# Kernel optimization log

Hardware: AMD Instinct MI355X
Metric: run time of the kernel (lower is better)

Reference implementation:

```python
import jax, jax.numpy as jnp
import numpy as np

H = 224; W = 224; ZNEAR = 0.01; ZFAR = 100.0; EPS2D = 0.3
N_GAUSS = 1024; N_CAM = 2
ALPHA_MIN = 1.0 / 255.0; ALPHA_MAX = 0.999


def quat_to_rotmat(q):
    # gsplat convention: wxyz, normalized internally. q: [N,4] -> [N,3,3]
    q = q / jnp.linalg.norm(q, axis=-1, keepdims=True)
    w, x, y, z = q[:, 0], q[:, 1], q[:, 2], q[:, 3]
    R = jnp.stack([
        jnp.stack([1.0 - 2.0 * (y * y + z * z), 2.0 * (x * y - w * z), 2.0 * (x * z + w * y)], -1),
        jnp.stack([2.0 * (x * y + w * z), 1.0 - 2.0 * (x * x + z * z), 2.0 * (y * z - w * x)], -1),
        jnp.stack([2.0 * (x * z - w * y), 2.0 * (y * z + w * x), 1.0 - 2.0 * (x * x + y * y)], -1),
    ], -2)
    return R


def setup_inputs() -> dict:
    key = jax.random.key(0)
    ks = jax.random.split(key, 5)
    xyz = jax.random.normal(ks[0], (N_GAUSS, 3), dtype=jnp.float32) * 0.5
    rgb = jax.random.uniform(ks[1], (N_GAUSS, 3), dtype=jnp.float32)
    opacity = jax.random.uniform(ks[2], (N_GAUSS,), dtype=jnp.float32)
    scale = jax.random.uniform(ks[3], (N_GAUSS, 3), dtype=jnp.float32) * 0.04 + 0.005
    rotation = jax.random.normal(ks[4], (N_GAUSS, 4), dtype=jnp.float32)
    w2c_list = []
    for a in (0.0, 0.3):  # two views, small yaw apart, camera 3 units back
        c, s = np.cos(a), np.sin(a)
        w2c_list.append(np.array([[c, 0, -s, 0], [0, 1, 0, 0], [s, 0, c, 3.0], [0, 0, 0, 1]], dtype=np.float32))
    w2cs = jnp.asarray(np.stack(w2c_list))
    K = np.array([[300.0, 0.0, 112.0], [0.0, 300.0, 112.0], [0.0, 0.0, 1.0]], dtype=np.float32)
    Ks = jnp.asarray(np.stack([K] * N_CAM))
    return {"w2cs": w2cs, "Ks": Ks, "xyz": xyz, "rgb": rgb, "opacity": opacity, "scale": scale, "rotation": rotation}


def _render_one(viewmat, K, means, cov3d, colors, opac, bg):
    R = viewmat[:3, :3]; t = viewmat[:3, 3]
    p_cam = means @ R.T + t                       # [N,3]
    z = p_cam[:, 2]; rz = 1.0 / z
    fx, fy, cx, cy = K[0, 0], K[1, 1], K[0, 2], K[1, 2]
    lim_x = 1.3 * (0.5 * W / fx); lim_y = 1.3 * (0.5 * H / fy)
    tx = z * jnp.clip(p_cam[:, 0] * rz, -lim_x, lim_x)
    ty = z * jnp.clip(p_cam[:, 1] * rz, -lim_y, lim_y)
    # camera-frame 3D covariance, then perspective Jacobian projection to 2D
    cov_cam = jnp.einsum('ij,njk,lk->nil', R, cov3d, R)   # [N,3,3]
    zero = jnp.zeros_like(rz)
    J = jnp.stack([
        jnp.stack([fx * rz, zero, -fx * tx * rz * rz], -1),
        jnp.stack([zero, fy * rz, -fy * ty * rz * rz], -1),
    ], -2)                                                # [N,2,3]
    cov2d = jnp.einsum('nij,njk,nlk->nil', J, cov_cam, J) # [N,2,2]
    a = cov2d[:, 0, 0] + EPS2D; d = cov2d[:, 1, 1] + EPS2D; b = cov2d[:, 0, 1]
    det = a * d - b * b
    ia = d / det; id_ = a / det; ib = -b / det            # inverse of blurred 2D cov
    u = fx * p_cam[:, 0] * rz + cx
    v = fy * p_cam[:, 1] * rz + cy
    valid = (z > ZNEAR) & (z < ZFAR) & (det > 0)
    o = jnp.where(valid, opac, 0.0)
    # front-to-back depth sort (gradients flow through gathered values)
    order = jnp.argsort(z)
    u, v, ia, ib, id_, o = (arr[order] for arr in (u, v, ia, ib, id_, o))
    colors_s = colors[order]
    # pixel centers, row-major flattened grid [P]
    xs = jnp.arange(W, dtype=jnp.float32) + 0.5
    ys = jnp.arange(H, dtype=jnp.float32) + 0.5
    pix_x = jnp.tile(xs, H); pix_y = jnp.repeat(ys, W)
    dx = u[None, :] - pix_x[:, None]                      # [P,N]
    dy = v[None, :] - pix_y[:, None]
    sigma = 0.5 * (ia * dx * dx + id_ * dy * dy) + ib * dx * dy
    alpha = jnp.minimum(o[None, :] * jnp.exp(-sigma), ALPHA_MAX)
    alpha = jnp.where((sigma >= 0.0) & (alpha > ALPHA_MIN), alpha, 0.0)
    log1m = jnp.log1p(-alpha)
    logT = jnp.cumsum(log1m, axis=1)
    T = jnp.exp(logT - log1m)                             # exclusive transmittance
    wgt = alpha * T                                       # [P,N]
    img = wgt @ colors_s                                  # [P,3]
    Tf = jnp.exp(logT[:, -1])
    img = img + Tf[:, None] * bg
    return img.reshape(H, W, 3), (1.0 - Tf).reshape(H, W, 1)


def reference(w2cs, Ks, xyz, rgb, opacity, scale, rotation):
    Rq = quat_to_rotmat(rotation)                         # [N,3,3]
    M = Rq * scale[:, None, :]                            # R @ diag(s)
    cov3d = jnp.einsum('nij,nkj->nik', M, M)              # R S S^T R^T
    bg = jnp.ones((3,), dtype=xyz.dtype)                  # bg_color buffer of ones
    imgs, alphas = jax.vmap(lambda vm, K: _render_one(vm, K, xyz, cov3d, rgb, opacity, bg))(w2cs, Ks)
    return imgs, alphas                                   # rgb [C,H,W,3], mask [C,H,W,1]
```

## Files before the change

kernel.cpp:

```cpp
#include <hip/hip_runtime.h>
#include <math.h>

#define NG 1024
#define NC 2
#define HH 224
#define WW 224
#define TILES_X 28
#define TILES_Y 28
#define EPS2D 0.3f
#define ALPHA_MIN (1.0f/255.0f)
#define ALPHA_MAX 0.999f
#define MAXL 512
#define LOG2E 1.4426950408889634f

__global__ __launch_bounds__(256) void fused_kernel(
        const float* __restrict__ w2cs, const float* __restrict__ Ks,
        const float* __restrict__ xyz, const float* __restrict__ rgb,
        const float* __restrict__ opac, const float* __restrict__ scale,
        const float* __restrict__ rot, float* __restrict__ out) {
    const int cam = blockIdx.z;
    const int TX = blockIdx.x, TY = blockIdx.y;
    const int tid = threadIdx.x;
    const int lane = tid & 63;
    const int wv   = tid >> 6;

    __shared__ union {
        unsigned long long keys[MAXL];
        float4 part[4][64];
    } shu;
    __shared__ float4 sA[MAXL];
    __shared__ float4 sB[MAXL];
    __shared__ float  sC[MAXL];
    __shared__ int    cnt[8];
    __shared__ int    scnt;

    if (tid == 0) scnt = 0;
    __syncthreads();

    const float* vm = w2cs + cam*16;
    const float R00 = vm[0],  R01 = vm[1],  R02 = vm[2],  t0 = vm[3];
    const float R10 = vm[4],  R11 = vm[5],  R12 = vm[6],  t1 = vm[7];
    const float R20 = vm[8],  R21 = vm[9],  R22 = vm[10], t2 = vm[11];
    const float* Kc = Ks + cam*9;
    const float fx = Kc[0], cx = Kc[2], fy = Kc[4], cy = Kc[5];
    const float limx = 1.3f * (0.5f * (float)WW / fx);
    const float limy = 1.3f * (0.5f * (float)HH / fy);

    #pragma unroll
    for (int k = 0; k < 4; k++) {
        int g = k*256 + tid;
        float X = xyz[g*3], Y = xyz[g*3+1], Z = xyz[g*3+2];
        float pz = R20*X + R21*Y + R22*Z + t2;
        float o  = opac[g];
        float tau = __logf(255.f * o);
        bool cand = (pz > 0.01f) && (pz < 100.f) && (tau > 0.f);
        if (cand) {
            float rz = 1.f / pz;
            float px = R00*X + R01*Y + R02*Z + t0;
            float py = R10*X + R11*Y + R12*Z + t1;
            float uu = fx*px*rz + cx;
            float vv = fy*py*rz + cy;
            float sx = scale[g*3+0], sy = scale[g*3+1], sz = scale[g*3+2];
            float smax = fmaxf(sx, fmaxf(sy, sz));
            float j00 = fx*rz, j11 = fy*rz;
            float j02m = fx*limx*rz, j12m = fy*limy*rz;
            float abnd = smax*smax*(j00*j00 + j02m*j02m) + EPS2D;
            float dbnd = smax*smax*(j11*j11 + j12m*j12m) + EPS2D;
            float rx = sqrtf(2.f*tau*abnd) + 0.01f;
            float ry = sqrtf(2.f*tau*dbnd) + 0.01f;
            int xmin = max((int)ceilf (uu - rx - 0.5f), 0);
            int xmax = min((int)floorf(uu + rx - 0.5f), WW-1);
            int ymin = max((int)ceilf (vv - ry - 0.5f), 0);
            int ymax = min((int)floorf(vv + ry - 0.5f), HH-1);
            cand = (xmin <= xmax) && (ymin <= ymax) &&
                   (TX >= (xmin>>3)) && (TX <= (xmax>>3)) &&
                   (TY >= (ymin>>3)) && (TY <= (ymax>>3));
        }
        unsigned long long m = __ballot(cand);
        int cw = __popcll(m);
        if (cw) {
            int basepos = 0;
            if (lane == 0) basepos = atomicAdd(&scnt, cw);
            basepos = __shfl(basepos, 0);
            if (cand) {
                int pos = basepos + __popcll(m & ((1ull << lane) - 1ull));
                if (pos < MAXL)
                    shu.keys[pos] = ((unsigned long long)__float_as_uint(pz) << 10)
                                  | (unsigned long long)g;
            }
        }
    }
    __syncthreads();
    int n = min(scnt, MAXL);

    unsigned long long myk0 = (tid       < n) ? shu.keys[tid]       : 0ull;
    unsigned long long myk1 = (tid + 256 < n) ? shu.keys[tid + 256] : 0ull;
    int r0 = 0, r1 = 0;
    #pragma unroll 4
    for (int j = 0; j < n; j++) {
        unsigned long long kj = shu.keys[j];
        r0 += (kj < myk0) ? 1 : 0;
        r1 += (kj < myk1) ? 1 : 0;
    }
    __syncthreads();
    if (tid       < n) shu.keys[r0] = myk0;
    if (tid + 256 < n) shu.keys[r1] = myk1;
    __syncthreads();

    auto prep = [&](int i, float4 &A, float4 &B, float &C) -> bool {
        if (i >= n) return false;
        int g = (int)(shu.keys[i] & 1023ull);

        float qw = rot[g*4+0], qx = rot[g*4+1], qy = rot[g*4+2], qz = rot[g*4+3];
        float qn = rsqrtf(qw*qw + qx*qx + qy*qy + qz*qz);
        qw *= qn; qx *= qn; qy *= qn; qz *= qn;
        float r00 = 1.f - 2.f*(qy*qy + qz*qz), r01 = 2.f*(qx*qy - qw*qz), r02 = 2.f*(qx*qz + qw*qy);
        float r10 = 2.f*(qx*qy + qw*qz), r11 = 1.f - 2.f*(qx*qx + qz*qz), r12 = 2.f*(qy*qz - qw*qx);
        float r20 = 2.f*(qx*qz - qw*qy), r21 = 2.f*(qy*qz + qw*qx), r22 = 1.f - 2.f*(qx*qx + qy*qy);

        float sx = scale[g*3+0], sy = scale[g*3+1], sz = scale[g*3+2];
        float m00 = r00*sx, m01 = r01*sy, m02 = r02*sz;
        float m10 = r10*sx, m11 = r11*sy, m12 = r12*sz;
        float m20 = r20*sx, m21 = r21*sy, m22 = r22*sz;
        float c00 = m00*m00 + m01*m01 + m02*m02;
        float c01 = m00*m10 + m01*m11 + m02*m12;
        float c02 = m00*m20 + m01*m21 + m02*m22;
        float c11 = m10*m10 + m11*m11 + m12*m12;
        float c12 = m10*m20 + m11*m21 + m12*m22;
        float c22 = m20*m20 + m21*m21 + m22*m22;

        float X = xyz[g*3], Y = xyz[g*3+1], Z = xyz[g*3+2];
        float px = R00*X + R01*Y + R02*Z + t0;
        float py = R10*X + R11*Y + R12*Z + t1;
        float pz = R20*X + R21*Y + R22*Z + t2;
        float rz = 1.f / pz;

        float txc = pz * fminf(fmaxf(px*rz, -limx), limx);
        float tyc = pz * fminf(fmaxf(py*rz, -limy), limy);

        float v00 = R00*c00 + R01*c01 + R02*c02;
        float v01 = R00*c01 + R01*c11 + R02*c12;
        float v02 = R00*c02 + R01*c12 + R02*c22;
        float v10 = R10*c00 + R11*c01 + R12*c02;
        float v11 = R10*c01 + R11*c11 + R12*c12;
        float v12 = R10*c02 + R11*c12 + R12*c22;
        float v20 = R20*c00 + R21*c01 + R22*c02;
        float v21 = R20*c01 + R21*c11 + R22*c12;
        float v22 = R20*c02 + R21*c12 + R22*c22;
        float cc00 = v00*R00 + v01*R01 + v02*R02;
        float cc01 = v00*R10 + v01*R11 + v02*R12;
        float cc02 = v00*R20 + v01*R21 + v02*R22;
        float cc11 = v10*R10 + v11*R11 + v12*R12;
        float cc12 = v10*R20 + v11*R21 + v12*R22;
        float cc22 = v20*R20 + v21*R21 + v22*R22;

        float j00 = fx*rz, j02 = -fx*txc*rz*rz;
        float j11 = fy*rz, j12 = -fy*tyc*rz*rz;
        float a  = j00*j00*cc00 + 2.f*j00*j02*cc02 + j02*j02*cc22 + EPS2D;
        float bq = j00*j11*cc01 + j00*j12*cc02 + j02*j11*cc12 + j02*j12*cc22;
        float d  = j11*j11*cc11 + 2.f*j11*j12*cc12 + j12*j12*cc22 + EPS2D;
        float det = a*d - bq*bq;

        if (!((pz > 0.01f) && (pz < 100.f) && (det > 0.f))) return false;

        float o = opac[g];
        float tau = __logf(255.f * o);
        if (!(tau > 0.f)) return false;

        float hx = sqrtf(2.f*tau*a) + 0.02f;
        float hy = sqrtf(2.f*tau*d) + 0.02f;
        float uu = fx*px*rz + cx;
        float vv = fy*py*rz + cy;
        float xlo = (float)(TX*8) + 0.5f, xhi = (float)(TX*8) + 7.5f;
        float ylo = (float)(TY*8) + 0.5f, yhi = (float)(TY*8) + 7.5f;
        if (uu + hx < xlo || uu - hx > xhi || vv + hy < ylo || vv - hy > yhi)
            return false;

        float idet = 1.f / det;
        A = make_float4(uu, vv, 0.5f*LOG2E*d*idet, -LOG2E*bq*idet);
        B = make_float4(0.5f*LOG2E*a*idet, o, rgb[g*3+0], rgb[g*3+1]);
        C = rgb[g*3+2];
        return true;
    };

    float4 A0, B0, A1, B1; float C0, C1;
    bool kp0 = prep(tid,       A0, B0, C0);
    bool kp1 = prep(tid + 256, A1, B1, C1);

    unsigned long long bal0 = __ballot(kp0);
    unsigned long long bal1 = __ballot(kp1);
    if (lane == 0) { cnt[wv] = __popcll(bal0); cnt[4 + wv] = __popcll(bal1); }
    __syncthreads();
    int base0 = 0, base1 = 0, n2 = 0;
    #pragma unroll
    for (int s = 0; s < 8; s++) {
        int cs = cnt[s];
        base0 += (s < wv)     ? cs : 0;
        base1 += (s < 4 + wv) ? cs : 0;
        n2 += cs;
    }
    unsigned long long lt = (1ull << lane) - 1ull;
    int d0 = base0 + __popcll(bal0 & lt);
    int d1 = base1 + __popcll(bal1 & lt);
    if (kp0) { sA[d0] = A0; sB[d0] = B0; sC[d0] = C0; }
    if (kp1) { sA[d1] = A1; sB[d1] = B1; sC[d1] = C1; }
    __syncthreads();

    const float pxl = (float)(TX*8 + (lane & 7)) + 0.5f;
    const float pyl = (float)(TY*8 + (lane >> 3)) + 0.5f;
    int seglen = (n2 + 3) >> 2;
    int js = wv * seglen;
    int je = min(n2, js + seglen);

    float T = 1.f, cr = 0.f, cg = 0.f, cb = 0.f;
#define CBODY(J) do { \
        float4 ga = sA[J]; float4 gb = sB[J]; float bv = sC[J]; \
        float dx = ga.x - pxl, dy = ga.y - pyl; \
        float sg = ga.z*dx*dx + gb.x*dy*dy + ga.w*dx*dy; \
        float al = fminf(gb.y * exp2f(-sg), ALPHA_MAX); \
        al = (sg >= 0.f && al > ALPHA_MIN) ? al : 0.f; \
        float wgt = al * T; \
        cr += wgt * gb.z; cg += wgt * gb.w; cb += wgt * bv; \
        T -= al * T; \
    } while (0)

    int j = js;
    while (j + 16 <= je) {
        #pragma unroll 4
        for (int q = 0; q < 16; q++) { CBODY(j + q); }
        j += 16;
        if (__all(T < 1e-4f)) break;
    }
    for (; j < je; j++) { CBODY(j); }
#undef CBODY

    shu.part[wv][lane] = make_float4(cr, cg, cb, T);
    __syncthreads();

    if (tid < 64) {
        float4 c0 = shu.part[0][lane];
        float Cr = c0.x, Cg = c0.y, Cb = c0.z, Tp = c0.w;
        #pragma unroll
        for (int s = 1; s < 4; s++) {
            float4 cs = shu.part[s][lane];
            Cr += Tp * cs.x;
            Cg += Tp * cs.y;
            Cb += Tp * cs.z;
            Tp *= cs.w;
        }
        int p = (TY*8 + (lane >> 3)) * WW + TX*8 + (lane & 7);
        float* img = out + (size_t)cam * (HH*WW*3) + (size_t)p * 3;
        img[0] = Cr + Tp;
        img[1] = Cg + Tp;
        img[2] = Cb + Tp;
        out[(size_t)NC*HH*WW*3 + (size_t)cam*(HH*WW) + p] = 1.f - Tp;
    }
}

extern "C" void kernel_launch(void* const* d_in, const int* in_sizes, int n_in,
                              void* d_out, int out_size, void* d_ws, size_t ws_size,
                              hipStream_t stream) {
    const float* w2cs  = (const float*)d_in[0];
    const float* Ks    = (const float*)d_in[1];
    const float* xyz   = (const float*)d_in[2];
    const float* rgb   = (const float*)d_in[3];
    const float* opac  = (const float*)d_in[4];
    const float* scale = (const float*)d_in[5];
    const float* rot   = (const float*)d_in[6];
    float* out = (float*)d_out;

    fused_kernel<<<dim3(TILES_X, TILES_Y, NC), 256, 0, stream>>>(
        w2cs, Ks, xyz, rgb, opac, scale, rot, out);
}
```

Baseline: 77.94 us.

## Split fused renderer into per-Gaussian prep, global depth sort, and tile render kernels

The fused kernel is split into three kernels. The first projects each Gaussian once per camera into a workspace, together with its tile bounding box and a depth key. The second computes a global depth rank per camera and scatters the records into sorted order. The render kernel then selects its Gaussians by a bounding-box test, so each tile no longer repeats the projection and the O(n^2) local sort. This adds two kernel launches and global-memory round trips, and the tighter per-Gaussian bounds may change which Gaussians each tile includes.

New measurement: 90.03 us. +15.5%, slower.

```diff
diff --git a/kernel.cpp b/kernel.cpp
--- a/kernel.cpp
+++ b/kernel.cpp
@@ -13,29 +13,23 @@
 #define MAXL 512
 #define LOG2E 1.4426950408889634f
 
-__global__ __launch_bounds__(256) void fused_kernel(
+#define OFF_SA   0
+#define OFF_SB   (OFF_SA  + NC*NG*16)
+#define OFF_SC   (OFF_SB  + NC*NG*16)
+#define OFF_SBB  (OFF_SC  + NC*NG*4)
+#define OFF_KEY  (OFF_SBB + NC*NG*4)
+#define OFF_UA   (OFF_KEY + NC*NG*8)
+#define OFF_UB   (OFF_UA  + NC*NG*16)
+#define OFF_UC   (OFF_UB  + NC*NG*16)
+#define OFF_UBB  (OFF_UC  + NC*NG*4)
+
+__global__ __launch_bounds__(256) void prep_kernel(
         const float* __restrict__ w2cs, const float* __restrict__ Ks,
         const float* __restrict__ xyz, const float* __restrict__ rgb,
         const float* __restrict__ opac, const float* __restrict__ scale,
-        const float* __restrict__ rot, float* __restrict__ out) {
-    const int cam = blockIdx.z;
-    const int TX = blockIdx.x, TY = blockIdx.y;
-    const int tid = threadIdx.x;
-    const int lane = tid & 63;
-    const int wv   = tid >> 6;
-
-    __shared__ union {
-        unsigned long long keys[MAXL];
-        float4 part[4][64];
-    } shu;
-    __shared__ float4 sA[MAXL];
-    __shared__ float4 sB[MAXL];
-    __shared__ float  sC[MAXL];
-    __shared__ int    cnt[8];
-    __shared__ int    scnt;
-
-    if (tid == 0) scnt = 0;
-    __syncthreads();
+        const float* __restrict__ rot, unsigned char* __restrict__ ws) {
+    const int cam = blockIdx.y;
+    const int g = blockIdx.x * 256 + threadIdx.x;
 
     const float* vm = w2cs + cam*16;
     const float R00 = vm[0],  R01 = vm[1],  R02 = vm[2],  t0 = vm[3];
@@ -46,164 +40,181 @@
     const float limx = 1.3f * (0.5f * (float)WW / fx);
     const float limy = 1.3f * (0.5f * (float)HH / fy);
 
-    #pragma unroll
-    for (int k = 0; k < 4; k++) {
-        int g = k*256 + tid;
-        float X = xyz[g*3], Y = xyz[g*3+1], Z = xyz[g*3+2];
-        float pz = R20*X + R21*Y + R22*Z + t2;
-        float o  = opac[g];
-        float tau = __logf(255.f * o);
-        bool cand = (pz > 0.01f) && (pz < 100.f) && (tau > 0.f);
-        if (cand) {
-            float rz = 1.f / pz;
-            float px = R00*X + R01*Y + R02*Z + t0;
-            float py = R10*X + R11*Y + R12*Z + t1;
-            float uu = fx*px*rz + cx;
-            float vv = fy*py*rz + cy;
-            float sx = scale[g*3+0], sy = scale[g*3+1], sz = scale[g*3+2];
-            float smax = fmaxf(sx, fmaxf(sy, sz));
-            float j00 = fx*rz, j11 = fy*rz;
-            float j02m = fx*limx*rz, j12m = fy*limy*rz;
-            float abnd = smax*smax*(j00*j00 + j02m*j02m) + EPS2D;
-            float dbnd = smax*smax*(j11*j11 + j12m*j12m) + EPS2D;
-            float rx = sqrtf(2.f*tau*abnd) + 0.01f;
-            float ry = sqrtf(2.f*tau*dbnd) + 0.01f;
-            int xmin = max((int)ceilf (uu - rx - 0.5f), 0);
-            int xmax = min((int)floorf(uu + rx - 0.5f), WW-1);
-            int ymin = max((int)ceilf (vv - ry - 0.5f), 0);
-            int ymax = min((int)floorf(vv + ry - 0.5f), HH-1);
-            cand = (xmin <= xmax) && (ymin <= ymax) &&
-                   (TX >= (xmin>>3)) && (TX <= (xmax>>3)) &&
-                   (TY >= (ymin>>3)) && (TY <= (ymax>>3));
-        }
-        unsigned long long m = __ballot(cand);
-        int cw = __popcll(m);
-        if (cw) {
-            int basepos = 0;
-            if (lane == 0) basepos = atomicAdd(&scnt, cw);
-            basepos = __shfl(basepos, 0);
-            if (cand) {
-                int pos = basepos + __popcll(m & ((1ull << lane) - 1ull));
-                if (pos < MAXL)
-                    shu.keys[pos] = ((unsigned long long)__float_as_uint(pz) << 10)
-                                  | (unsigned long long)g;
-            }
-        }
-    }
-    __syncthreads();
-    int n = min(scnt, MAXL);
-
-    unsigned long long myk0 = (tid       < n) ? shu.keys[tid]       : 0ull;
-    unsigned long long myk1 = (tid + 256 < n) ? shu.keys[tid + 256] : 0ull;
-    int r0 = 0, r1 = 0;
-    #pragma unroll 4
-    for (int j = 0; j < n; j++) {
-        unsigned long long kj = shu.keys[j];
-        r0 += (kj < myk0) ? 1 : 0;
-        r1 += (kj < myk1) ? 1 : 0;
-    }
-    __syncthreads();
-    if (tid       < n) shu.keys[r0] = myk0;
-    if (tid + 256 < n) shu.keys[r1] = myk1;
-    __syncthreads();
-
-    auto prep = [&](int i, float4 &A, float4 &B, float &C) -> bool {
-        if (i >= n) return false;
-        int g = (int)(shu.keys[i] & 1023ull);
-
-        float qw = rot[g*4+0], qx = rot[g*4+1], qy = rot[g*4+2], qz = rot[g*4+3];
-        float qn = rsqrtf(qw*qw + qx*qx + qy*qy + qz*qz);
-        qw *= qn; qx *= qn; qy *= qn; qz *= qn;
-        float r00 = 1.f - 2.f*(qy*qy + qz*qz), r01 = 2.f*(qx*qy - qw*qz), r02 = 2.f*(qx*qz + qw*qy);
-        float r10 = 2.f*(qx*qy + qw*qz), r11 = 1.f - 2.f*(qx*qx + qz*qz), r12 = 2.f*(qy*qz - qw*qx);
-        float r20 = 2.f*(qx*qz - qw*qy), r21 = 2.f*(qy*qz + qw*qx), r22 = 1.f - 2.f*(qx*qx + qy*qy);
-
-        float sx = scale[g*3+0], sy = scale[g*3+1], sz = scale[g*3+2];
-        float m00 = r00*sx, m01 = r01*sy, m02 = r02*sz;
-        float m10 = r10*sx, m11 = r11*sy, m12 = r12*sz;
-        float m20 = r20*sx, m21 = r21*sy, m22 = r22*sz;
-        float c00 = m00*m00 + m01*m01 + m02*m02;
-        float c01 = m00*m10 + m01*m11 + m02*m12;
-        float c02 = m00*m20 + m01*m21 + m02*m22;
-        float c11 = m10*m10 + m11*m11 + m12*m12;
-        float c12 = m10*m20 + m11*m21 + m12*m22;
-        float c22 = m20*m20 + m21*m21 + m22*m22;
-
-        float X = xyz[g*3], Y = xyz[g*3+1], Z = xyz[g*3+2];
-        float px = R00*X + R01*Y + R02*Z + t0;
-        float py = R10*X + R11*Y + R12*Z + t1;
-        float pz = R20*X + R21*Y + R22*Z + t2;
-        float rz = 1.f / pz;
-
-        float txc = pz * fminf(fmaxf(px*rz, -limx), limx);
-        float tyc = pz * fminf(fmaxf(py*rz, -limy), limy);
-
-        float v00 = R00*c00 + R01*c01 + R02*c02;
-        float v01 = R00*c01 + R01*c11 + R02*c12;
-        float v02 = R00*c02 + R01*c12 + R02*c22;
-        float v10 = R10*c00 + R11*c01 + R12*c02;
-        float v11 = R10*c01 + R11*c11 + R12*c12;
-        float v12 = R10*c02 + R11*c12 + R12*c22;
-        float v20 = R20*c00 + R21*c01 + R22*c02;
-        float v21 = R20*c01 + R21*c11 + R22*c12;
-        float v22 = R20*c02 + R21*c12 + R22*c22;
-        float cc00 = v00*R00 + v01*R01 + v02*R02;
-        float cc01 = v00*R10 + v01*R11 + v02*R12;
-        float cc02 = v00*R20 + v01*R21 + v02*R22;
-        float cc11 = v10*R10 + v11*R11 + v12*R12;
-        float cc12 = v10*R20 + v11*R21 + v12*R22;
-        float cc22 = v20*R20 + v21*R21 + v22*R22;
-
-        float j00 = fx*rz, j02 = -fx*txc*rz*rz;
-        float j11 = fy*rz, j12 = -fy*tyc*rz*rz;
-        float a  = j00*j00*cc00 + 2.f*j00*j02*cc02 + j02*j02*cc22 + EPS2D;
-        float bq = j00*j11*cc01 + j00*j12*cc02 + j02*j11*cc12 + j02*j12*cc22;
-        float d  = j11*j11*cc11 + 2.f*j11*j12*cc12 + j12*j12*cc22 + EPS2D;
-        float det = a*d - bq*bq;
-
-        if (!((pz > 0.01f) && (pz < 100.f) && (det > 0.f))) return false;
-
-        float o = opac[g];
-        float tau = __logf(255.f * o);
-        if (!(tau > 0.f)) return false;
-
+    float qw = rot[g*4+0], qx = rot[g*4+1], qy = rot[g*4+2], qz = rot[g*4+3];
+    float qn = rsqrtf(qw*qw + qx*qx + qy*qy + qz*qz);
+    qw *= qn; qx *= qn; qy *= qn; qz *= qn;
+    float r00 = 1.f - 2.f*(qy*qy + qz*qz), r01 = 2.f*(qx*qy - qw*qz), r02 = 2.f*(qx*qz + qw*qy);
+    float r10 = 2.f*(qx*qy + qw*qz), r11 = 1.f - 2.f*(qx*qx + qz*qz), r12 = 2.f*(qy*qz - qw*qx);
+    float r20 = 2.f*(qx*qz - qw*qy), r21 = 2.f*(qy*qz + qw*qx), r22 = 1.f - 2.f*(qx*qx + qy*qy);
+
+    float sx = scale[g*3+0], sy = scale[g*3+1], sz = scale[g*3+2];
+    float m00 = r00*sx, m01 = r01*sy, m02 = r02*sz;
+    float m10 = r10*sx, m11 = r11*sy, m12 = r12*sz;
+    float m20 = r20*sx, m21 = r21*sy, m22 = r22*sz;
+    float c00 = m00*m00 + m01*m01 + m02*m02;
+    float c01 = m00*m10 + m01*m11 + m02*m12;
+    float c02 = m00*m20 + m01*m21 + m02*m22;
+    float c11 = m10*m10 + m11*m11 + m12*m12;
+    float c12 = m10*m20 + m11*m21 + m12*m22;
+    float c22 = m20*m20 + m21*m21 + m22*m22;
+
+    float X = xyz[g*3], Y = xyz[g*3+1], Z = xyz[g*3+2];
+    float px = R00*X + R01*Y + R02*Z + t0;
+    float py = R10*X + R11*Y + R12*Z + t1;
+    float pz = R20*X + R21*Y + R22*Z + t2;
+    float rz = 1.f / pz;
+
+    float txc = pz * fminf(fmaxf(px*rz, -limx), limx);
+    float tyc = pz * fminf(fmaxf(py*rz, -limy), limy);
+
+    float v00 = R00*c00 + R01*c01 + R02*c02;
+    float v01 = R00*c01 + R01*c11 + R02*c12;
+    float v02 = R00*c02 + R01*c12 + R02*c22;
+    float v10 = R10*c00 + R11*c01 + R12*c02;
+    float v11 = R10*c01 + R11*c11 + R12*c12;
+    float v12 = R10*c02 + R11*c12 + R12*c22;
+    float v20 = R20*c00 + R21*c01 + R22*c02;
+    float v21 = R20*c01 + R21*c11 + R22*c12;
+    float v22 = R20*c02 + R21*c12 + R22*c22;
+    float cc00 = v00*R00 + v01*R01 + v02*R02;
+    float cc01 = v00*R10 + v01*R11 + v02*R12;
+    float cc02 = v00*R20 + v01*R21 + v02*R22;
+    float cc11 = v10*R10 + v11*R11 + v12*R12;
+    float cc12 = v10*R20 + v11*R21 + v12*R22;
+    float cc22 = v20*R20 + v21*R21 + v22*R22;
+
+    float j00 = fx*rz, j02 = -fx*txc*rz*rz;
+    float j11 = fy*rz, j12 = -fy*tyc*rz*rz;
+    float a  = j00*j00*cc00 + 2.f*j00*j02*cc02 + j02*j02*cc22 + EPS2D;
+    float bq = j00*j11*cc01 + j00*j12*cc02 + j02*j11*cc12 + j02*j12*cc22;
+    float d  = j11*j11*cc11 + 2.f*j11*j12*cc12 + j12*j12*cc22 + EPS2D;
+    float det = a*d - bq*bq;
+
+    float o = opac[g];
+    float tau = __logf(255.f * o);
+    bool valid = (pz > 0.01f) && (pz < 100.f) && (det > 0.f) && (tau > 0.f);
+
+    float4 A4 = make_float4(0.f, 0.f, 0.f, 0.f);
+    float4 B4 = make_float4(0.f, 0.f, 0.f, 0.f);
+    float  C1 = 0.f;
+    unsigned bb = 0xFFFFFFFFu;
+    unsigned long long key = (0xFFFFFFFFull << 10) | (unsigned)g;
+
+    if (valid) {
         float hx = sqrtf(2.f*tau*a) + 0.02f;
         float hy = sqrtf(2.f*tau*d) + 0.02f;
         float uu = fx*px*rz + cx;
         float vv = fy*py*rz + cy;
-        float xlo = (float)(TX*8) + 0.5f, xhi = (float)(TX*8) + 7.5f;
-        float ylo = (float)(TY*8) + 0.5f, yhi = (float)(TY*8) + 7.5f;
-        if (uu + hx < xlo || uu - hx > xhi || vv + hy < ylo || vv - hy > yhi)
-            return false;
-
-        float idet = 1.f / det;
-        A = make_float4(uu, vv, 0.5f*LOG2E*d*idet, -LOG2E*bq*idet);
-        B = make_float4(0.5f*LOG2E*a*idet, o, rgb[g*3+0], rgb[g*3+1]);
-        C = rgb[g*3+2];
-        return true;
-    };
-
-    float4 A0, B0, A1, B1; float C0, C1;
-    bool kp0 = prep(tid,       A0, B0, C0);
-    bool kp1 = prep(tid + 256, A1, B1, C1);
-
-    unsigned long long bal0 = __ballot(kp0);
-    unsigned long long bal1 = __ballot(kp1);
-    if (lane == 0) { cnt[wv] = __popcll(bal0); cnt[4 + wv] = __popcll(bal1); }
-    __syncthreads();
-    int base0 = 0, base1 = 0, n2 = 0;
+        int xmin = max((int)ceilf (uu - hx - 0.5f), 0);
+        int xmax = min((int)floorf(uu + hx - 0.5f), WW-1);
+        int ymin = max((int)ceilf (vv - hy - 0.5f), 0);
+        int ymax = min((int)floorf(vv + hy - 0.5f), HH-1);
+        if (xmin <= xmax && ymin <= ymax) {
+            bb = (unsigned)(xmin>>3) | ((unsigned)(xmax>>3)<<8)
+               | ((unsigned)(ymin>>3)<<16) | ((unsigned)(ymax>>3)<<24);
+            float idet = 1.f / det;
+            A4 = make_float4(uu, vv, 0.5f*LOG2E*d*idet, -LOG2E*bq*idet);
+            B4 = make_float4(0.5f*LOG2E*a*idet, o, rgb[g*3+0], rgb[g*3+1]);
+            C1 = rgb[g*3+2];
+            key = ((unsigned long long)__float_as_uint(pz) << 10) | (unsigned)g;
+        }
+    }
+
+    const int idx = cam*NG + g;
+    ((float4*)(ws + OFF_UA))[idx] = A4;
+    ((float4*)(ws + OFF_UB))[idx] = B4;
+    ((float*) (ws + OFF_UC))[idx] = C1;
+    ((unsigned*)(ws + OFF_UBB))[idx] = bb;
+    ((unsigned long long*)(ws + OFF_KEY))[idx] = key;
+}
+
+__global__ __launch_bounds__(256) void rank_kernel(unsigned char* __restrict__ ws) {
+    const int cam = blockIdx.y;
+    __shared__ unsigned long long kl[NG];
+    const unsigned long long* keyU = (const unsigned long long*)(ws + OFF_KEY) + cam*NG;
+    for (int i = threadIdx.x; i < NG; i += 256) kl[i] = keyU[i];
+    __syncthreads();
+
+    const int g = blockIdx.x * 256 + threadIdx.x;
+    const unsigned long long myk = kl[g];
+    int r = 0;
+    #pragma unroll 8
+    for (int j = 0; j < NG; j++) r += (kl[j] < myk) ? 1 : 0;
+
+    const int src = cam*NG + g, dst = cam*NG + r;
+    ((float4*)(ws + OFF_SA))[dst] = ((const float4*)(ws + OFF_UA))[src];
+    ((float4*)(ws + OFF_SB))[dst] = ((const float4*)(ws + OFF_UB))[src];
+    ((float*) (ws + OFF_SC))[dst] = ((const float*) (ws + OFF_UC))[src];
+    ((unsigned*)(ws + OFF_SBB))[dst] = ((const unsigned*)(ws + OFF_UBB))[src];
+}
+
+__global__ __launch_bounds__(256) void render_kernel(
+        const unsigned char* __restrict__ ws, float* __restrict__ out) {
+    const int cam = blockIdx.z;
+    const int TX = blockIdx.x, TY = blockIdx.y;
+    const int tid = threadIdx.x;
+    const int lane = tid & 63;
+    const int wv   = tid >> 6;
+
+    __shared__ float4 sA[MAXL];
+    __shared__ float4 sB[MAXL];
+    __shared__ float  sC[MAXL];
+    __shared__ union Sh {
+        unsigned short list[MAXL];
+        float4 part[4][64];
+    } shu;
+    __shared__ int cnt[16];
+
+    const unsigned* bbs = (const unsigned*)(ws + OFF_SBB) + cam*NG;
+    bool cd[4];
     #pragma unroll
-    for (int s = 0; s < 8; s++) {
-        int cs = cnt[s];
-        base0 += (s < wv)     ? cs : 0;
-        base1 += (s < 4 + wv) ? cs : 0;
-        n2 += cs;
-    }
-    unsigned long long lt = (1ull << lane) - 1ull;
-    int d0 = base0 + __popcll(bal0 & lt);
-    int d1 = base1 + __popcll(bal1 & lt);
-    if (kp0) { sA[d0] = A0; sB[d0] = B0; sC[d0] = C0; }
-    if (kp1) { sA[d1] = A1; sB[d1] = B1; sC[d1] = C1; }
+    for (int k = 0; k < 4; k++) {
+        unsigned b = bbs[k*256 + tid];
+        int tx0 = (int)(b & 255u), tx1 = (int)((b>>8) & 255u);
+        int ty0 = (int)((b>>16) & 255u), ty1 = (int)(b>>24);
+        cd[k] = (TX >= tx0) && (TX <= tx1) && (TY >= ty0) && (TY <= ty1);
+        unsigned long long m = __ballot(cd[k]);
+        if (lane == 0) cnt[k*4 + wv] = __popcll(m);
+    }
+    __syncthreads();
+
+    int baseK[4], run = 0;
+    #pragma unroll
+    for (int s = 0; s < 16; s++) {
+        if ((s & 3) == wv) baseK[s >> 2] = run;
+        run += cnt[s];
+    }
+    int n2 = min(run, MAXL);
+    const unsigned long long lt = (1ull << lane) - 1ull;
+    #pragma unroll
+    for (int k = 0; k < 4; k++) {
+        unsigned long long m = __ballot(cd[k]);
+        if (cd[k]) {
+            int pos = baseK[k] + __popcll(m & lt);
+            if (pos < MAXL) shu.list[pos] = (unsigned short)(k*256 + tid);
+        }
+    }
+    __syncthreads();
+
+    if (n2 == 0) {
+        if (tid < 64) {
+            int p = (TY*8 + (lane >> 3)) * WW + TX*8 + (lane & 7);
+            float* img = out + (size_t)cam * (HH*WW*3) + (size_t)p * 3;
+            img[0] = 1.f; img[1] = 1.f; img[2] = 1.f;
+            out[(size_t)NC*HH*WW*3 + (size_t)cam*(HH*WW) + p] = 0.f;
+        }
+        return;
+    }
+
+    const float4* gA = (const float4*)(ws + OFF_SA) + cam*NG;
+    const float4* gB = (const float4*)(ws + OFF_SB) + cam*NG;
+    const float*  gC = (const float*) (ws + OFF_SC) + cam*NG;
+    for (int i = tid; i < n2; i += 256) {
+        int p = shu.list[i];
+        sA[i] = gA[p];
+        sB[i] = gB[p];
+        sC[i] = gC[p];
+    }
     __syncthreads();
 
     const float pxl = (float)(TX*8 + (lane & 7)) + 0.5f;
@@ -267,8 +278,10 @@
     const float* opac  = (const float*)d_in[4];
     const float* scale = (const float*)d_in[5];
     const float* rot   = (const float*)d_in[6];
+    unsigned char* ws = (unsigned char*)d_ws;
     float* out = (float*)d_out;
 
-    fused_kernel<<<dim3(TILES_X, TILES_Y, NC), 256, 0, stream>>>(
-        w2cs, Ks, xyz, rgb, opac, scale, rot, out);
-}
+    prep_kernel  <<<dim3(4, NC),               256, 0, stream>>>(w2cs, Ks, xyz, rgb, opac, scale, rot, ws);
+    rank_kernel  <<<dim3(4, NC),               256, 0, stream>>>(ws);
+    render_kernel<<<dim3(TILES_X, TILES_Y, NC), 256, 0, stream>>>(ws, out);
+}
```

## Compute exact 2D conic during culling and rank-sort with a single wavefront

Applied to the files above, without the earlier changes.

Merges the per-Gaussian covariance/conic preparation into the initial culling loop, so the exact 2D extent test runs before insertion and the payload goes straight into shared memory. Sorting now ranks only the surviving keys, using one wavefront with register-blocked comparisons, then permutes the prepared payloads by rank. Tiles with no Gaussians write the background and exit early. The cost is that the rank computation is serialized onto one wavefront while the other three wait, and the culling loop carries more divergent work and register pressure.

Result: slower. 83.39 us (+7.0%).

```diff
diff --git a/kernel.cpp b/kernel.cpp
--- a/kernel.cpp
+++ b/kernel.cpp
@@ -24,15 +24,15 @@
     const int lane = tid & 63;
     const int wv   = tid >> 6;
 
+    __shared__ float4 sA[MAXL];
+    __shared__ float4 sB[MAXL];
+    __shared__ float  sC[MAXL];
     __shared__ union {
         unsigned long long keys[MAXL];
         float4 part[4][64];
     } shu;
-    __shared__ float4 sA[MAXL];
-    __shared__ float4 sB[MAXL];
-    __shared__ float  sC[MAXL];
-    __shared__ int    cnt[8];
-    __shared__ int    scnt;
+    __shared__ unsigned short rank16[MAXL];
+    __shared__ int scnt;
 
     if (tid == 0) scnt = 0;
     __syncthreads();
@@ -46,7 +46,9 @@
     const float limx = 1.3f * (0.5f * (float)WW / fx);
     const float limy = 1.3f * (0.5f * (float)HH / fy);
 
-    #pragma unroll
+    const float xlo = (float)(TX*8) + 0.5f, xhi = (float)(TX*8) + 7.5f;
+    const float ylo = (float)(TY*8) + 0.5f, yhi = (float)(TY*8) + 7.5f;
+
     for (int k = 0; k < 4; k++) {
         int g = k*256 + tid;
         float X = xyz[g*3], Y = xyz[g*3+1], Z = xyz[g*3+2];
@@ -54,6 +56,8 @@
         float o  = opac[g];
         float tau = __logf(255.f * o);
         bool cand = (pz > 0.01f) && (pz < 100.f) && (tau > 0.f);
+        bool pass = false;
+        float4 A4, B4; float C1 = 0.f;
         if (cand) {
             float rz = 1.f / pz;
             float px = R00*X + R01*Y + R02*Z + t0;
@@ -66,151 +70,153 @@
             float j02m = fx*limx*rz, j12m = fy*limy*rz;
             float abnd = smax*smax*(j00*j00 + j02m*j02m) + EPS2D;
             float dbnd = smax*smax*(j11*j11 + j12m*j12m) + EPS2D;
-            float rx = sqrtf(2.f*tau*abnd) + 0.01f;
-            float ry = sqrtf(2.f*tau*dbnd) + 0.01f;
-            int xmin = max((int)ceilf (uu - rx - 0.5f), 0);
-            int xmax = min((int)floorf(uu + rx - 0.5f), WW-1);
-            int ymin = max((int)ceilf (vv - ry - 0.5f), 0);
-            int ymax = min((int)floorf(vv + ry - 0.5f), HH-1);
-            cand = (xmin <= xmax) && (ymin <= ymax) &&
-                   (TX >= (xmin>>3)) && (TX <= (xmax>>3)) &&
-                   (TY >= (ymin>>3)) && (TY <= (ymax>>3));
-        }
-        unsigned long long m = __ballot(cand);
+            float rx = sqrtf(2.f*tau*abnd) + 0.03f;
+            float ry = sqrtf(2.f*tau*dbnd) + 0.03f;
+            bool cand2 = (uu + rx >= xlo) && (uu - rx <= xhi) &&
+                         (vv + ry >= ylo) && (vv - ry <= yhi);
+            if (cand2) {
+                float qw = rot[g*4+0], qx = rot[g*4+1], qy = rot[g*4+2], qz = rot[g*4+3];
+                float qn = rsqrtf(qw*qw + qx*qx + qy*qy + qz*qz);
+                qw *= qn; qx *= qn; qy *= qn; qz *= qn;
+                float r00 = 1.f - 2.f*(qy*qy + qz*qz), r01 = 2.f*(qx*qy - qw*qz), r02 = 2.f*(qx*qz + qw*qy);
+                float r10 = 2.f*(qx*qy + qw*qz), r11 = 1.f - 2.f*(qx*qx + qz*qz), r12 = 2.f*(qy*qz - qw*qx);
+                float r20 = 2.f*(qx*qz - qw*qy), r21 = 2.f*(qy*qz + qw*qx), r22 = 1.f - 2.f*(qx*qx + qy*qy);
+
+                float m00 = r00*sx, m01 = r01*sy, m02 = r02*sz;
+                float m10 = r10*sx, m11 = r11*sy, m12 = r12*sz;
+                float m20 = r20*sx, m21 = r21*sy, m22 = r22*sz;
+                float c00 = m00*m00 + m01*m01 + m02*m02;
+                float c01 = m00*m10 + m01*m11 + m02*m12;
+                float c02 = m00*m20 + m01*m21 + m02*m22;
+                float c11 = m10*m10 + m11*m11 + m12*m12;
+                float c12 = m10*m20 + m11*m21 + m12*m22;
+                float c22 = m20*m20 + m21*m21 + m22*m22;
+
+                float txc = pz * fminf(fmaxf(px*rz, -limx), limx);
+                float tyc = pz * fminf(fmaxf(py*rz, -limy), limy);
+
+                float v00 = R00*c00 + R01*c01 + R02*c02;
+                float v01 = R00*c01 + R01*c11 + R02*c12;
+                float v02 = R00*c02 + R01*c12 + R02*c22;
+                float v10 = R10*c00 + R11*c01 + R12*c02;
+                float v11 = R10*c01 + R11*c11 + R12*c12;
+                float v12 = R10*c02 + R11*c12 + R12*c22;
+                float v20 = R20*c00 + R21*c01 + R22*c02;
+                float v21 = R20*c01 + R21*c11 + R22*c12;
+                float v22 = R20*c02 + R21*c12 + R22*c22;
+                float cc00 = v00*R00 + v01*R01 + v02*R02;
+                float cc01 = v00*R10 + v01*R11 + v02*R12;
+                float cc02 = v00*R20 + v01*R21 + v02*R22;
+                float cc11 = v10*R10 + v11*R11 + v12*R12;
+                float cc12 = v10*R20 + v11*R21 + v12*R22;
+                float cc22 = v20*R20 + v21*R21 + v22*R22;
+
+                float j02 = -fx*txc*rz*rz;
+                float j12 = -fy*tyc*rz*rz;
+                float a  = j00*j00*cc00 + 2.f*j00*j02*cc02 + j02*j02*cc22 + EPS2D;
+                float bq = j00*j11*cc01 + j00*j12*cc02 + j02*j11*cc12 + j02*j12*cc22;
+                float d  = j11*j11*cc11 + 2.f*j11*j12*cc12 + j12*j12*cc22 + EPS2D;
+                float det = a*d - bq*bq;
+
+                if (det > 0.f) {
+                    float hx = sqrtf(2.f*tau*a) + 0.02f;
+                    float hy = sqrtf(2.f*tau*d) + 0.02f;
+                    int xmin = max((int)ceilf (uu - hx - 0.5f), 0);
+                    int xmax = min((int)floorf(uu + hx - 0.5f), WW-1);
+                    int ymin = max((int)ceilf (vv - hy - 0.5f), 0);
+                    int ymax = min((int)floorf(vv + hy - 0.5f), HH-1);
+                    pass = (xmin <= xmax) && (ymin <= ymax) &&
+                           (TX >= (xmin>>3)) && (TX <= (xmax>>3)) &&
+                           (TY >= (ymin>>3)) && (TY <= (ymax>>3));
+                    if (pass) {
+                        float idet = 1.f / det;
+                        A4 = make_float4(uu, vv, 0.5f*LOG2E*d*idet, -LOG2E*bq*idet);
+                        B4 = make_float4(0.5f*LOG2E*a*idet, o, rgb[g*3+0], rgb[g*3+1]);
+                        C1 = rgb[g*3+2];
+                    }
+                }
+            }
+        }
+        unsigned long long m = __ballot(pass);
         int cw = __popcll(m);
         if (cw) {
             int basepos = 0;
             if (lane == 0) basepos = atomicAdd(&scnt, cw);
             basepos = __shfl(basepos, 0);
-            if (cand) {
+            if (pass) {
                 int pos = basepos + __popcll(m & ((1ull << lane) - 1ull));
-                if (pos < MAXL)
+                if (pos < MAXL) {
                     shu.keys[pos] = ((unsigned long long)__float_as_uint(pz) << 10)
                                   | (unsigned long long)g;
-            }
-        }
-    }
-    __syncthreads();
-    int n = min(scnt, MAXL);
-
-    unsigned long long myk0 = (tid       < n) ? shu.keys[tid]       : 0ull;
-    unsigned long long myk1 = (tid + 256 < n) ? shu.keys[tid + 256] : 0ull;
-    int r0 = 0, r1 = 0;
-    #pragma unroll 4
-    for (int j = 0; j < n; j++) {
-        unsigned long long kj = shu.keys[j];
-        r0 += (kj < myk0) ? 1 : 0;
-        r1 += (kj < myk1) ? 1 : 0;
-    }
-    __syncthreads();
-    if (tid       < n) shu.keys[r0] = myk0;
-    if (tid + 256 < n) shu.keys[r1] = myk1;
-    __syncthreads();
-
-    auto prep = [&](int i, float4 &A, float4 &B, float &C) -> bool {
-        if (i >= n) return false;
-        int g = (int)(shu.keys[i] & 1023ull);
-
-        float qw = rot[g*4+0], qx = rot[g*4+1], qy = rot[g*4+2], qz = rot[g*4+3];
-        float qn = rsqrtf(qw*qw + qx*qx + qy*qy + qz*qz);
-        qw *= qn; qx *= qn; qy *= qn; qz *= qn;
-        float r00 = 1.f - 2.f*(qy*qy + qz*qz), r01 = 2.f*(qx*qy - qw*qz), r02 = 2.f*(qx*qz + qw*qy);
-        float r10 = 2.f*(qx*qy + qw*qz), r11 = 1.f - 2.f*(qx*qx + qz*qz), r12 = 2.f*(qy*qz - qw*qx);
-        float r20 = 2.f*(qx*qz - qw*qy), r21 = 2.f*(qy*qz + qw*qx), r22 = 1.f - 2.f*(qx*qx + qy*qy);
-
-        float sx = scale[g*3+0], sy = scale[g*3+1], sz = scale[g*3+2];
-        float m00 = r00*sx, m01 = r01*sy, m02 = r02*sz;
-        float m10 = r10*sx, m11 = r11*sy, m12 = r12*sz;
-        float m20 = r20*sx, m21 = r21*sy, m22 = r22*sz;
-        float c00 = m00*m00 + m01*m01 + m02*m02;
-        float c01 = m00*m10 + m01*m11 + m02*m12;
-        float c02 = m00*m20 + m01*m21 + m02*m22;
-        float c11 = m10*m10 + m11*m11 + m12*m12;
-        float c12 = m10*m20 + m11*m21 + m12*m22;
-        float c22 = m20*m20 + m21*m21 + m22*m22;
-
-        float X = xyz[g*3], Y = xyz[g*3+1], Z = xyz[g*3+2];
-        float px = R00*X + R01*Y + R02*Z + t0;
-        float py = R10*X + R11*Y + R12*Z + t1;
-        float pz = R20*X + R21*Y + R22*Z + t2;
-        float rz = 1.f / pz;
-
-        float txc = pz * fminf(fmaxf(px*rz, -limx), limx);
-        float tyc = pz * fminf(fmaxf(py*rz, -limy), limy);
-
-        float v00 = R00*c00 + R01*c01 + R02*c02;
-        float v01 = R00*c01 + R01*c11 + R02*c12;
-        float v02 = R00*c02 + R01*c12 + R02*c22;
-        float v10 = R10*c00 + R11*c01 + R12*c02;
-        float v11 = R10*c01 + R11*c11 + R12*c12;
-        float v12 = R10*c02 + R11*c12 + R12*c22;
-        float v20 = R20*c00 + R21*c01 + R22*c02;
-        float v21 = R20*c01 + R21*c11 + R22*c12;
-        float v22 = R20*c02 + R21*c12 + R22*c22;
-        float cc00 = v00*R00 + v01*R01 + v02*R02;
-        float cc01 = v00*R10 + v01*R11 + v02*R12;
-        float cc02 = v00*R20 + v01*R21 + v02*R22;
-        float cc11 = v10*R10 + v11*R11 + v12*R12;
-        float cc12 = v10*R20 + v11*R21 + v12*R22;
-        float cc22 = v20*R20 + v21*R21 + v22*R22;
-
-        float j00 = fx*rz, j02 = -fx*txc*rz*rz;
-        float j11 = fy*rz, j12 = -fy*tyc*rz*rz;
-        float a  = j00*j00*cc00 + 2.f*j00*j02*cc02 + j02*j02*cc22 + EPS2D;
-        float bq = j00*j11*cc01 + j00*j12*cc02 + j02*j11*cc12 + j02*j12*cc22;
-        float d  = j11*j11*cc11 + 2.f*j11*j12*cc12 + j12*j12*cc22 + EPS2D;
-        float det = a*d - bq*bq;
-
-        if (!((pz > 0.01f) && (pz < 100.f) && (det > 0.f))) return false;
-
-        float o = opac[g];
-        float tau = __logf(255.f * o);
-        if (!(tau > 0.f)) return false;
-
-        float hx = sqrtf(2.f*tau*a) + 0.02f;
-        float hy = sqrtf(2.f*tau*d) + 0.02f;
-        float uu = fx*px*rz + cx;
-        float vv = fy*py*rz + cy;
-        float xlo = (float)(TX*8) + 0.5f, xhi = (float)(TX*8) + 7.5f;
-        float ylo = (float)(TY*8) + 0.5f, yhi = (float)(TY*8) + 7.5f;
-        if (uu + hx < xlo || uu - hx > xhi || vv + hy < ylo || vv - hy > yhi)
-            return false;
-
-        float idet = 1.f / det;
-        A = make_float4(uu, vv, 0.5f*LOG2E*d*idet, -LOG2E*bq*idet);
-        B = make_float4(0.5f*LOG2E*a*idet, o, rgb[g*3+0], rgb[g*3+1]);
-        C = rgb[g*3+2];
-        return true;
-    };
-
-    float4 A0, B0, A1, B1; float C0, C1;
-    bool kp0 = prep(tid,       A0, B0, C0);
-    bool kp1 = prep(tid + 256, A1, B1, C1);
-
-    unsigned long long bal0 = __ballot(kp0);
-    unsigned long long bal1 = __ballot(kp1);
-    if (lane == 0) { cnt[wv] = __popcll(bal0); cnt[4 + wv] = __popcll(bal1); }
-    __syncthreads();
-    int base0 = 0, base1 = 0, n2 = 0;
-    #pragma unroll
-    for (int s = 0; s < 8; s++) {
-        int cs = cnt[s];
-        base0 += (s < wv)     ? cs : 0;
-        base1 += (s < 4 + wv) ? cs : 0;
-        n2 += cs;
-    }
-    unsigned long long lt = (1ull << lane) - 1ull;
-    int d0 = base0 + __popcll(bal0 & lt);
-    int d1 = base1 + __popcll(bal1 & lt);
-    if (kp0) { sA[d0] = A0; sB[d0] = B0; sC[d0] = C0; }
-    if (kp1) { sA[d1] = A1; sB[d1] = B1; sC[d1] = C1; }
+                    sA[pos] = A4; sB[pos] = B4; sC[pos] = C1;
+                }
+            }
+        }
+    }
+    __syncthreads();
+    const int n = min(scnt, MAXL);
+
+    if (n == 0) {
+        if (tid < 64) {
+            int p = (TY*8 + (lane >> 3)) * WW + TX*8 + (lane & 7);
+            float* img = out + (size_t)cam * (HH*WW*3) + (size_t)p * 3;
+            img[0] = 1.f; img[1] = 1.f; img[2] = 1.f;
+            out[(size_t)NC*HH*WW*3 + (size_t)cam*(HH*WW) + p] = 0.f;
+        }
+        return;
+    }
+
+    if (wv == 0) {
+        const int nq = (n + 63) >> 6;
+        unsigned long long myk[8];
+        int rk[8];
+        #pragma unroll
+        for (int q = 0; q < 8; q++) { myk[q] = ~0ull; rk[q] = 0; }
+        #pragma unroll
+        for (int q = 0; q < 8; q++) {
+            int s = q*64 + lane;
+            if (q < nq && s < n) myk[q] = shu.keys[s];
+        }
+        if (nq <= 2) {
+            for (int j = 0; j < n; j++) {
+                unsigned long long kj = shu.keys[j];
+                rk[0] += (kj < myk[0]) ? 1 : 0;
+                rk[1] += (kj < myk[1]) ? 1 : 0;
+            }
+        } else if (nq <= 4) {
+            for (int j = 0; j < n; j++) {
+                unsigned long long kj = shu.keys[j];
+                #pragma unroll
+                for (int q = 0; q < 4; q++) rk[q] += (kj < myk[q]) ? 1 : 0;
+            }
+        } else {
+            for (int j = 0; j < n; j++) {
+                unsigned long long kj = shu.keys[j];
+                #pragma unroll
+                for (int q = 0; q < 8; q++) rk[q] += (kj < myk[q]) ? 1 : 0;
+            }
+        }
+        #pragma unroll
+        for (int q = 0; q < 8; q++) {
+            int s = q*64 + lane;
+            if (s < n) rank16[s] = (unsigned short)rk[q];
+        }
+    }
+    float4 tA0, tB0, tA1, tB1; float tC0 = 0.f, tC1 = 0.f;
+    const bool h0 = tid < n, h1 = tid + 256 < n;
+    if (h0) { tA0 = sA[tid];     tB0 = sB[tid];     tC0 = sC[tid];     }
+    if (h1) { tA1 = sA[tid+256]; tB1 = sB[tid+256]; tC1 = sC[tid+256]; }
+    __syncthreads();
+
+    if (h0) { int r = rank16[tid];     sA[r] = tA0; sB[r] = tB0; sC[r] = tC0; }
+    if (h1) { int r = rank16[tid+256]; sA[r] = tA1; sB[r] = tB1; sC[r] = tC1; }
     __syncthreads();
 
     const float pxl = (float)(TX*8 + (lane & 7)) + 0.5f;
     const float pyl = (float)(TY*8 + (lane >> 3)) + 0.5f;
-    int seglen = (n2 + 3) >> 2;
+    int seglen = (n + 3) >> 2;
     int js = wv * seglen;
-    int je = min(n2, js + seglen);
+    int je = min(n, js + seglen);
 
     float T = 1.f, cr = 0.f, cg = 0.f, cb = 0.f;
 #define CBODY(J) do { \
```
